# Kernel tuning notes

Hardware: AMD Instinct MI355X
Metric: run time of the kernel (lower is better)

## Reference

```python
import jax, jax.numpy as jnp
import numpy as np

EMBED = 1024
HEADS = 16
HEAD_DIM = EMBED // HEADS


def setup_inputs() -> dict:
    key = jax.random.key(0)
    ks = jax.random.split(key, 6)
    scale = 1.0 / np.sqrt(EMBED)
    x = jax.random.normal(ks[0], (2, 2048, EMBED), dtype=jnp.float32)
    # nn.Linear weights stored as [out_features, in_features]
    Wq = jax.random.normal(ks[1], (EMBED, EMBED), dtype=jnp.float32) * scale
    Wk = jax.random.normal(ks[2], (EMBED, EMBED), dtype=jnp.float32) * scale
    Wv = jax.random.normal(ks[3], (EMBED, EMBED), dtype=jnp.float32) * scale
    Wo = jax.random.normal(ks[4], (EMBED, EMBED), dtype=jnp.float32) * scale
    bo = jax.random.normal(ks[5], (EMBED,), dtype=jnp.float32) * scale
    return {"x": x, "Wq": Wq, "Wk": Wk, "Wv": Wv, "Wo": Wo, "bo": bo}


def reference(x, Wq, Wk, Wv, Wo, bo):
    N, L, E = x.shape
    # projections (torch Linear: x @ W.T)
    q = (x @ Wq.T).reshape(N, L, HEADS, HEAD_DIM).transpose(0, 2, 1, 3)  # [N,H,L,D]
    k = (x @ Wk.T).reshape(N, L, HEADS, HEAD_DIM).transpose(0, 2, 1, 3)
    v = (x @ Wv.T).reshape(N, L, HEADS, HEAD_DIM).transpose(0, 2, 1, 3)
    # scores scaled by sqrt(embed_size) (as in source, not sqrt(head_dim))
    scores = jnp.einsum("nhqd,nhkd->nhqk", q, k) / jnp.sqrt(jnp.float32(E))
    attn = jax.nn.softmax(scores, axis=-1)
    out = jnp.einsum("nhqk,nhkd->nhqd", attn, v)  # [N,H,L,D]
    out = out.transpose(0, 2, 1, 3).reshape(N, L, E)
    return out @ Wo.T + bo
```

## Files before the change

kernel.cpp:

```cpp
#include <hip/hip_runtime.h>
#include <hip/hip_bf16.h>

constexpr int NB  = 2;
constexpr int SL  = 2048;
constexpr int EMB = 1024;
constexpr int NH  = 16;
constexpr int HD  = 64;
constexpr int MT  = NB * SL;
constexpr size_t PROJ = (size_t)MT * EMB;

typedef __attribute__((ext_vector_type(8))) short bf16x8;
typedef __attribute__((ext_vector_type(4))) float f32x4;

__device__ inline short f2b(float f) {
  __hip_bfloat16 b = __float2bfloat16(f);
  short s; __builtin_memcpy(&s, &b, 2); return s;
}

#define GLDS16(g, l)                                                     \
  __builtin_amdgcn_global_load_lds(                                      \
      (const __attribute__((address_space(1))) void*)(g),                \
      (__attribute__((address_space(3))) void*)(l), 16, 0, 0)

__global__ __launch_bounds__(256) void cast_all(
    const float* __restrict__ x,  const float* __restrict__ wq,
    const float* __restrict__ wk, const float* __restrict__ wv,
    const float* __restrict__ wo, short* __restrict__ xb,
    short* __restrict__ wqkv, short* __restrict__ wob) {
  const size_t t = (size_t)blockIdx.x * 256 + threadIdx.x;
  const float* src; short* dst; size_t base;
  if (t < 1048576)      { src = x;  dst = xb;              base = 0; }
  else if (t < 1310720) { src = wq; dst = wqkv;            base = 1048576; }
  else if (t < 1572864) { src = wk; dst = wqkv + (1 << 20); base = 1310720; }
  else if (t < 1835008) { src = wv; dst = wqkv + (2 << 20); base = 1572864; }
  else                  { src = wo; dst = wob;             base = 1835008; }
  const size_t i = t - base;
  const float4 v = ((const float4*)src)[i];
  const short4 o = {f2b(v.x), f2b(v.y), f2b(v.z), f2b(v.w)};
  ((short4*)dst)[i] = o;
}

__global__ __launch_bounds__(256) void gemm_qkv(
    const short* __restrict__ A, const short* __restrict__ W,
    short* __restrict__ qb, short* __restrict__ kb, short* __restrict__ vt) {
  __shared__ short As[128 * 64];
  __shared__ short Bs[128 * 64];
  const int tid = threadIdx.x;
  const int w = tid >> 6, lane = tid & 63;
  const int la = lane >> 4, lb = lane & 15;
  const int wm = w & 1, wn = w >> 1;
  const int m0 = blockIdx.y << 7, n0 = blockIdx.x << 7;
  const int srow = lane >> 3;
  const int scol = ((lane & 7) ^ srow) << 3;
  const short* a0 = A + (size_t)(m0 + w * 32 + srow) * 1024 + scol;
  const short* b0 = W + (size_t)(n0 + w * 32 + srow) * 1024 + scol;
  short* lAw = As + (w * 32) * 64;
  short* lBw = Bs + (w * 32) * 64;

  f32x4 acc[4][4];
#pragma unroll
  for (int i = 0; i < 4; ++i)
#pragma unroll
    for (int j = 0; j < 4; ++j) acc[i][j] = (f32x4){0.f, 0.f, 0.f, 0.f};

  for (int k0 = 0; k0 < 1024; k0 += 64) {
    __syncthreads();
#pragma unroll
    for (int g = 0; g < 4; ++g) GLDS16(a0 + g * 8 * 1024 + k0, lAw + g * 8 * 64);
#pragma unroll
    for (int g = 0; g < 4; ++g) GLDS16(b0 + g * 8 * 1024 + k0, lBw + g * 8 * 64);
    __syncthreads();
#pragma unroll
    for (int ks = 0; ks < 2; ++ks) {
      bf16x8 af[4], bfr[4];
#pragma unroll
      for (int i = 0; i < 4; ++i) {
        const int row = wm * 64 + i * 16 + lb;
        af[i] = *(const bf16x8*)&As[row * 64 + (((ks << 2) + la) ^ (row & 7)) * 8];
      }
#pragma unroll
      for (int j = 0; j < 4; ++j) {
        const int row = wn * 64 + j * 16 + lb;
        bfr[j] = *(const bf16x8*)&Bs[row * 64 + (((ks << 2) + la) ^ (row & 7)) * 8];
      }
#pragma unroll
      for (int i = 0; i < 4; ++i)
#pragma unroll
        for (int j = 0; j < 4; ++j)
          acc[i][j] = __builtin_amdgcn_mfma_f32_16x16x32_bf16(af[i], bfr[j],
                                                              acc[i][j], 0, 0, 0);
    }
  }

  const int region = n0 >> 10;
  if (region == 0) {
    const float sc = 0.03125f * 1.44269504f;
#pragma unroll
    for (int j = 0; j < 4; ++j) {
      const int nj = (n0 & 1023) + wn * 64 + j * 16 + lb;
#pragma unroll
      for (int i = 0; i < 4; ++i) {
        const int mi = m0 + wm * 64 + i * 16 + la * 4;
#pragma unroll
        for (int r = 0; r < 4; ++r)
          qb[(size_t)(mi + r) * 1024 + nj] = f2b(acc[i][j][r] * sc);
      }
    }
  } else if (region == 1) {
#pragma unroll
    for (int j = 0; j < 4; ++j) {
      const int nj = (n0 & 1023) + wn * 64 + j * 16 + lb;
      const int hh = nj >> 6, d = nj & 63;
      const int ks = d >> 5, Gd = (d >> 3) & 3, jj = d & 7;
#pragma unroll
      for (int i = 0; i < 4; ++i) {
        const int mi = m0 + wm * 64 + i * 16 + la * 4;
        const int nbi = mi >> 11, seq = mi & (SL - 1);
        const size_t base = ((size_t)(nbi * NH + hh) << 17) +
                            (size_t)(seq >> 4) * 1024 + ks * 512 + Gd * 128 +
                            (seq & 15) * 8 + jj;
#pragma unroll
        for (int r = 0; r < 4; ++r) kb[base + r * 8] = f2b(acc[i][j][r]);
      }
    }
  } else {
#pragma unroll
    for (int j = 0; j < 4; ++j) {
      const int nv = (n0 - 2048) + wn * 64 + j * 16 + lb;
      const int hh = nv >> 6, d = nv & 63;
      const int mtd = d >> 4, lbv = d & 15;
#pragma unroll
      for (int i = 0; i < 4; ++i) {
        const int mi = m0 + wm * 64 + i * 16 + la * 4;
        const int nbi = mi >> 11, seq = mi & (SL - 1);
        const int kq = seq >> 5, g = (seq >> 2) & 3, hi = (seq >> 4) & 1;
        const short4 o = {f2b(acc[i][j][0]), f2b(acc[i][j][1]),
                          f2b(acc[i][j][2]), f2b(acc[i][j][3])};
        *(short4*)&vt[((size_t)(nbi * NH + hh) << 17) + (size_t)kq * 2048 +
                      mtd * 512 + g * 128 + lbv * 8 + 4 * hi] = o;
      }
    }
  }
}

__global__ __launch_bounds__(256) void gemm_out(
    const short* __restrict__ A, const short* __restrict__ W,
    const float* __restrict__ bias, float* __restrict__ out) {
  __shared__ short As[128 * 64];
  __shared__ short Bs[64 * 64];
  const int tid = threadIdx.x;
  const int w = tid >> 6, lane = tid & 63;
  const int la = lane >> 4, lb = lane & 15;
  const int wm = w & 1, wn = w >> 1;
  const int m0 = blockIdx.y << 7, n0 = blockIdx.x << 6;
  const int srow = lane >> 3;
  const int scol = ((lane & 7) ^ srow) << 3;
  const short* a0 = A + (size_t)(m0 + w * 32 + srow) * 1024 + scol;
  const short* b0 = W + (size_t)(n0 + w * 16 + srow) * 1024 + scol;
  short* lAw = As + (w * 32) * 64;
  short* lBw = Bs + (w * 16) * 64;

  f32x4 acc[4][2];
#pragma unroll
  for (int i = 0; i < 4; ++i)
#pragma unroll
    for (int j = 0; j < 2; ++j) acc[i][j] = (f32x4){0.f, 0.f, 0.f, 0.f};

  for (int k0 = 0; k0 < 1024; k0 += 64) {
    __syncthreads();
#pragma unroll
    for (int g = 0; g < 4; ++g) GLDS16(a0 + g * 8 * 1024 + k0, lAw + g * 8 * 64);
#pragma unroll
    for (int g = 0; g < 2; ++g) GLDS16(b0 + g * 8 * 1024 + k0, lBw + g * 8 * 64);
    __syncthreads();
#pragma unroll
    for (int ks = 0; ks < 2; ++ks) {
      bf16x8 af[4], bfr[2];
#pragma unroll
      for (int i = 0; i < 4; ++i) {
        const int row = wm * 64 + i * 16 + lb;
        af[i] = *(const bf16x8*)&As[row * 64 + (((ks << 2) + la) ^ (row & 7)) * 8];
      }
#pragma unroll
      for (int j = 0; j < 2; ++j) {
        const int row = wn * 32 + j * 16 + lb;
        bfr[j] = *(const bf16x8*)&Bs[row * 64 + (((ks << 2) + la) ^ (row & 7)) * 8];
      }
#pragma unroll
      for (int i = 0; i < 4; ++i)
#pragma unroll
        for (int j = 0; j < 2; ++j)
          acc[i][j] = __builtin_amdgcn_mfma_f32_16x16x32_bf16(af[i], bfr[j],
                                                              acc[i][j], 0, 0, 0);
    }
  }
#pragma unroll
  for (int j = 0; j < 2; ++j) {
    const int nj = n0 + wn * 32 + j * 16 + lb;
    const float bv = bias[nj];
#pragma unroll
    for (int i = 0; i < 4; ++i) {
      const int mi = m0 + wm * 64 + i * 16 + la * 4;
#pragma unroll
      for (int r = 0; r < 4; ++r)
        out[(size_t)(mi + r) * 1024 + nj] = acc[i][j][r] + bv;
    }
  }
}

#define LOADK(DK, KB32)                                                      \
  do {                                                                       \
    _Pragma("unroll") for (int rr_ = 0; rr_ < 2; ++rr_)                      \
        _Pragma("unroll") for (int ks_ = 0; ks_ < 2; ++ks_)                  \
            DK[rr_][ks_] = *(const bf16x8*)(Kb + (size_t)(KB32) * 2048 +     \
                                            rr_ * 1024 + ks_ * 512);         \
  } while (0)

#define LOADV(DV, KB32)                                                      \
  do {                                                                       \
    _Pragma("unroll") for (int md_ = 0; md_ < 4; ++md_)                      \
        DV[md_] = *(const bf16x8*)(Vb + (size_t)(KB32) * 2048 + md_ * 512);  \
  } while (0)

#define ATTN_STEP(AK, AV)                                                    \
  do {                                                                       \
    f32x4 S[2][4];                                                           \
    _Pragma("unroll") for (int mt = 0; mt < 2; ++mt)                         \
        _Pragma("unroll") for (int nt = 0; nt < 4; ++nt)                     \
            S[mt][nt] = (f32x4){0.f, 0.f, 0.f, 0.f};                         \
    __builtin_amdgcn_s_setprio(1);                                           \
    _Pragma("unroll") for (int ks = 0; ks < 2; ++ks)                         \
        _Pragma("unroll") for (int nt = 0; nt < 4; ++nt) {                   \
      S[0][nt] = __builtin_amdgcn_mfma_f32_16x16x32_bf16(AK[0][ks],          \
                     bQ[nt][ks], S[0][nt], 0, 0, 0);                         \
      S[1][nt] = __builtin_amdgcn_mfma_f32_16x16x32_bf16(AK[1][ks],          \
                     bQ[nt][ks], S[1][nt], 0, 0, 0);                         \
    }                                                                        \
    __builtin_amdgcn_s_setprio(0);                                           \
    _Pragma("unroll") for (int nt = 0; nt < 4; ++nt) {                       \
      _Pragma("unroll") for (int mt = 0; mt < 2; ++mt)                       \
          _Pragma("unroll") for (int r = 0; r < 4; ++r) {                    \
        const float p = __builtin_amdgcn_exp2f(S[mt][nt][r]);                \
        S[mt][nt][r] = p;                                                    \
        lacc[nt] += p;                                                       \
      }                                                                      \
      bf16x8 B2;                                                             \
      B2[0] = f2b(S[0][nt][0]); B2[1] = f2b(S[0][nt][1]);                    \
      B2[2] = f2b(S[0][nt][2]); B2[3] = f2b(S[0][nt][3]);                    \
      B2[4] = f2b(S[1][nt][0]); B2[5] = f2b(S[1][nt][1]);                    \
      B2[6] = f2b(S[1][nt][2]); B2[7] = f2b(S[1][nt][3]);                    \
      __builtin_amdgcn_s_setprio(1);                                         \
      _Pragma("unroll") for (int mtd = 0; mtd < 4; ++mtd)                    \
          O[mtd][nt] = __builtin_amdgcn_mfma_f32_16x16x32_bf16(              \
              AV[mtd], B2, O[mtd][nt], 0, 0, 0);                             \
      __builtin_amdgcn_s_setprio(0);                                         \
    }                                                                        \
  } while (0)

__global__ __launch_bounds__(256, 2) void attn_mfma(const short* __restrict__ Qg,
                                                    const short* __restrict__ Kp,
                                                    const short* __restrict__ Vp,
                                                    short* __restrict__ Ab) {
  __shared__ __align__(16) float red[2][64][68];
  __shared__ float lred[128];
  const int tid = threadIdx.x;
  const int w = tid >> 6, lane = tid & 63;
  const int G = lane >> 4, lb = lane & 15;
  const int wk = w & 1, wq = w >> 1;
  const int h = blockIdx.x, qt = blockIdx.y, n = blockIdx.z;

  const short* Qb = Qg + ((size_t)(n * SL + (qt << 7) + 64 * wq)) * EMB + h * HD;
  bf16x8 bQ[4][2];
#pragma unroll
  for (int nt = 0; nt < 4; ++nt)
#pragma unroll
    for (int ks = 0; ks < 2; ++ks)
      bQ[nt][ks] =
          *(const bf16x8*)(Qb + (size_t)(16 * nt + lb) * EMB + 32 * ks + 8 * G);

  f32x4 O[4][4];
  float lacc[4] = {0.f, 0.f, 0.f, 0.f};
#pragma unroll
  for (int i = 0; i < 4; ++i)
#pragma unroll
    for (int j = 0; j < 4; ++j) O[i][j] = (f32x4){0.f, 0.f, 0.f, 0.f};

  const short* Kb = Kp + (((size_t)(n * NH + h)) << 17) + lane * 8;
  const short* Vb = Vp + (((size_t)(n * NH + h)) << 17) + lane * 8;

  bf16x8 K0[2][2], V0[4], K1[2][2], V1[4];
  LOADK(K0, 2 * wk);
  LOADV(V0, 2 * wk);
  for (int it = 0; it < 32; it += 2) {
    const int kA = 2 * it + 2 * wk;
    LOADK(K1, kA + 1);
    LOADV(V1, kA + 1);
    ATTN_STEP(K0, V0);
    if (it + 2 < 32) {
      LOADK(K0, kA + 4);
      LOADV(V0, kA + 4);
    }
    ATTN_STEP(K1, V1);
  }

#pragma unroll
  for (int nt = 0; nt < 4; ++nt) {
    lacc[nt] += __shfl_xor(lacc[nt], 16);
    lacc[nt] += __shfl_xor(lacc[nt], 32);
  }

  if (wk == 1) {
#pragma unroll
    for (int nt = 0; nt < 4; ++nt) {
      const int q = 16 * nt + lb;
#pragma unroll
      for (int mtd = 0; mtd < 4; ++mtd)
        *(f32x4*)&red[wq][q][16 * mtd + 4 * G] = O[mtd][nt];
      if (G == 0) lred[wq * 64 + q] = lacc[nt];
    }
  }
  __syncthreads();
  if (wk == 0) {
    short* Ao = Ab + ((size_t)(n * SL + (qt << 7) + 64 * wq)) * EMB + h * HD;
#pragma unroll
    for (int nt = 0; nt < 4; ++nt) {
      const int q = 16 * nt + lb;
      const float inv = 1.f / (lacc[nt] + lred[wq * 64 + q]);
#pragma unroll
      for (int mtd = 0; mtd < 4; ++mtd) {
        const f32x4 t = *(const f32x4*)&red[wq][q][16 * mtd + 4 * G];
        const f32x4 s = t + O[mtd][nt];
        const short4 o = {f2b(s[0] * inv), f2b(s[1] * inv), f2b(s[2] * inv),
                          f2b(s[3] * inv)};
        *(short4*)(Ao + (size_t)q * EMB + 16 * mtd + 4 * G) = o;
      }
    }
  }
}

extern "C" void kernel_launch(void* const* d_in, const int* in_sizes, int n_in,
                              void* d_out, int out_size, void* d_ws, size_t ws_size,
                              hipStream_t stream) {
  const float* x  = (const float*)d_in[0];
  const float* Wq = (const float*)d_in[1];
  const float* Wk = (const float*)d_in[2];
  const float* Wv = (const float*)d_in[3];
  const float* Wo = (const float*)d_in[4];
  const float* bo = (const float*)d_in[5];
  float* out = (float*)d_out;

  short* xb   = (short*)d_ws;
  short* wqkv = xb + PROJ;
  short* wob  = wqkv + 3u * EMB * EMB;
  short* qb   = wob + (size_t)EMB * EMB;
  short* kb   = qb + PROJ;
  short* vt   = kb + PROJ;
  short* ab   = qb;

  cast_all<<<8192, 256, 0, stream>>>(x, Wq, Wk, Wv, Wo, xb, wqkv, wob);
  gemm_qkv<<<dim3(24, 32), 256, 0, stream>>>(xb, wqkv, qb, kb, vt);
  attn_mfma<<<dim3(NH, SL / 128, NB), 256, 0, stream>>>(qb, kb, vt, ab);
  gemm_out<<<dim3(16, 32), 256, 0, stream>>>(ab, wob, bo, out);
}
```

Before: 174.0 us.

## Rewrite QKV GEMM as 256x256 tile double-buffered pipeline with 8 waves

The QKV projection GEMM moves from 128x128 tiles with 4 waves and a single LDS buffer to 256x256 tiles with 8 waves, 128 KB of dynamic LDS double-buffering, and half-tile async global-to-LDS loads interleaved with MFMA groups under manual waitcnt and barriers. It also swizzles block order and raises wave priority around MFMA bursts. The aim is to hide load latency and improve operand reuse. The cost is a large LDS footprint and only 192 blocks, which may leave CUs underfilled, and the hand-placed waits carry a correctness risk.

```diff
diff --git a/kernel.cpp b/kernel.cpp
--- a/kernel.cpp
+++ b/kernel.cpp
@@ -40,56 +40,138 @@
   ((short4*)dst)[i] = o;
 }
 
-__global__ __launch_bounds__(256) void gemm_qkv(
+#define QBAR() asm volatile("s_barrier" ::: "memory")
+#define QVM(n) asm volatile("s_waitcnt vmcnt(" #n ")" ::: "memory")
+
+#define STAGEH(gh, lh)                                                   \
+  do {                                                                   \
+    GLDS16((gh) + go0, (lh) + w16 * 64);                                 \
+    GLDS16((gh) + go1, (lh) + w16 * 64 + 512);                           \
+  } while (0)
+
+#define LDAQ(pa, ks)                                                     \
+  _Pragma("unroll") for (int i_ = 0; i_ < 8; ++i_)                       \
+      aR[i_] = *(const bf16x8*)&(pa)[(wm128 + i_ * 16 + lb) * 64 +       \
+                                     ((((ks) << 2) + G) ^ lb7) * 8];
+
+#define LDBQ(dst, pb, j0, ks)                                            \
+  dst[0] = *(const bf16x8*)&(pb)[(wn64 + (j0) * 16 + lb) * 64 +          \
+                                 ((((ks) << 2) + G) ^ lb7) * 8];         \
+  dst[1] = *(const bf16x8*)&(pb)[(wn64 + ((j0) + 1) * 16 + lb) * 64 +    \
+                                 ((((ks) << 2) + G) ^ lb7) * 8];
+
+#define MMQ(bp, j0)                                                      \
+  __builtin_amdgcn_s_setprio(1);                                         \
+  _Pragma("unroll") for (int i_ = 0; i_ < 8; ++i_) {                     \
+    acc[i_][j0] = __builtin_amdgcn_mfma_f32_16x16x32_bf16(               \
+        aR[i_], bp[0], acc[i_][j0], 0, 0, 0);                            \
+    acc[i_][(j0) + 1] = __builtin_amdgcn_mfma_f32_16x16x32_bf16(         \
+        aR[i_], bp[1], acc[i_][(j0) + 1], 0, 0, 0);                      \
+  }                                                                      \
+  __builtin_amdgcn_s_setprio(0);
+
+__global__ __launch_bounds__(512, 2) void gemm_qkv(
     const short* __restrict__ A, const short* __restrict__ W,
     short* __restrict__ qb, short* __restrict__ kb, short* __restrict__ vt) {
-  __shared__ short As[128 * 64];
-  __shared__ short Bs[128 * 64];
+  extern __shared__ short lds[];
   const int tid = threadIdx.x;
   const int w = tid >> 6, lane = tid & 63;
-  const int la = lane >> 4, lb = lane & 15;
-  const int wm = w & 1, wn = w >> 1;
-  const int m0 = blockIdx.y << 7, n0 = blockIdx.x << 7;
-  const int srow = lane >> 3;
-  const int scol = ((lane & 7) ^ srow) << 3;
-  const short* a0 = A + (size_t)(m0 + w * 32 + srow) * 1024 + scol;
-  const short* b0 = W + (size_t)(n0 + w * 32 + srow) * 1024 + scol;
-  short* lAw = As + (w * 32) * 64;
-  short* lBw = Bs + (w * 32) * 64;
-
-  f32x4 acc[4][4];
-#pragma unroll
-  for (int i = 0; i < 4; ++i)
+  const int G = lane >> 4, lb = lane & 15, lb7 = lb & 7;
+  const int wm = w >> 2, wn = w & 3;
+  const int wm128 = wm * 128, wn64 = wn * 64;
+  const int bid = blockIdx.x;
+  const int swz = (bid & 7) * 24 + (bid >> 3);
+  const int by = swz / 12, bx = swz % 12;
+  const int m0 = by << 8, n0 = bx << 8;
+  const int w16 = w * 16;
+  const int lr = lane >> 3;
+  const int lc = ((lane & 7) ^ lr) << 3;
+  const size_t go0 = (size_t)(w16 + lr) * 1024 + lc;
+  const size_t go1 = go0 + (size_t)8 * 1024;
+  const short* aH0 = A + (size_t)m0 * 1024;
+  const short* aH1 = A + (size_t)(m0 + 128) * 1024;
+  const short* bH0 = W + (size_t)n0 * 1024;
+  const short* bH1 = W + (size_t)(n0 + 128) * 1024;
+  short* a0s = lds;
+  short* b0s = lds + 16384;
+  short* a1s = lds + 32768;
+  short* b1s = lds + 49152;
+
+  f32x4 acc[8][4];
+#pragma unroll
+  for (int i = 0; i < 8; ++i)
 #pragma unroll
     for (int j = 0; j < 4; ++j) acc[i][j] = (f32x4){0.f, 0.f, 0.f, 0.f};
-
-  for (int k0 = 0; k0 < 1024; k0 += 64) {
-    __syncthreads();
-#pragma unroll
-    for (int g = 0; g < 4; ++g) GLDS16(a0 + g * 8 * 1024 + k0, lAw + g * 8 * 64);
-#pragma unroll
-    for (int g = 0; g < 4; ++g) GLDS16(b0 + g * 8 * 1024 + k0, lBw + g * 8 * 64);
-    __syncthreads();
-#pragma unroll
-    for (int ks = 0; ks < 2; ++ks) {
-      bf16x8 af[4], bfr[4];
-#pragma unroll
-      for (int i = 0; i < 4; ++i) {
-        const int row = wm * 64 + i * 16 + lb;
-        af[i] = *(const bf16x8*)&As[row * 64 + (((ks << 2) + la) ^ (row & 7)) * 8];
-      }
-#pragma unroll
-      for (int j = 0; j < 4; ++j) {
-        const int row = wn * 64 + j * 16 + lb;
-        bfr[j] = *(const bf16x8*)&Bs[row * 64 + (((ks << 2) + la) ^ (row & 7)) * 8];
-      }
-#pragma unroll
-      for (int i = 0; i < 4; ++i)
-#pragma unroll
-        for (int j = 0; j < 4; ++j)
-          acc[i][j] = __builtin_amdgcn_mfma_f32_16x16x32_bf16(af[i], bfr[j],
-                                                              acc[i][j], 0, 0, 0);
-    }
+  bf16x8 aR[8], b01[2], b23[2];
+
+  STAGEH(aH0, a0s);
+  STAGEH(aH1, a0s + 8192);
+  STAGEH(bH0, b0s);
+  STAGEH(bH1, b0s + 8192);
+  STAGEH(aH0 + 64, a1s);
+  STAGEH(aH1 + 64, a1s + 8192);
+  STAGEH(bH0 + 64, b1s);
+  STAGEH(bH1 + 64, b1s + 8192);
+  QVM(8);
+  QBAR();
+
+  for (int it = 0; it < 7; ++it) {
+    const size_t k1 = (size_t)(2 * it + 1) * 64;
+    const size_t k2 = (size_t)(2 * it + 2) * 64;
+    const size_t k3 = (size_t)(2 * it + 3) * 64;
+    LDAQ(a0s, 0);
+    LDBQ(b01, b0s, 0, 0);
+    if (it > 0) STAGEH(aH1 + k1, a1s + 8192);
+    QBAR(); MMQ(b01, 0); QBAR();
+    LDBQ(b23, b0s, 2, 0);
+    if (it > 0) STAGEH(bH0 + k1, b1s);
+    QBAR(); MMQ(b23, 2); QBAR();
+    LDAQ(a0s, 1);
+    LDBQ(b01, b0s, 0, 1);
+    if (it > 0) STAGEH(bH1 + k1, b1s + 8192);
+    QBAR(); MMQ(b01, 0); QBAR();
+    LDBQ(b23, b0s, 2, 1);
+    STAGEH(aH0 + k2, a0s);
+    QVM(2);
+    QBAR(); MMQ(b23, 2); QBAR();
+    LDAQ(a1s, 0);
+    LDBQ(b01, b1s, 0, 0);
+    STAGEH(aH1 + k2, a0s + 8192);
+    QBAR(); MMQ(b01, 0); QBAR();
+    LDBQ(b23, b1s, 2, 0);
+    STAGEH(bH0 + k2, b0s);
+    QBAR(); MMQ(b23, 2); QBAR();
+    LDAQ(a1s, 1);
+    LDBQ(b01, b1s, 0, 1);
+    STAGEH(bH1 + k2, b0s + 8192);
+    QBAR(); MMQ(b01, 0); QBAR();
+    LDBQ(b23, b1s, 2, 1);
+    STAGEH(aH0 + k3, a1s);
+    QVM(2);
+    QBAR(); MMQ(b23, 2); QBAR();
+  }
+  {
+    const size_t k1 = (size_t)15 * 64;
+    LDAQ(a0s, 0); LDBQ(b01, b0s, 0, 0);
+    STAGEH(aH1 + k1, a1s + 8192);
+    QBAR(); MMQ(b01, 0); QBAR();
+    LDBQ(b23, b0s, 2, 0);
+    STAGEH(bH0 + k1, b1s);
+    QBAR(); MMQ(b23, 2); QBAR();
+    LDAQ(a0s, 1); LDBQ(b01, b0s, 0, 1);
+    STAGEH(bH1 + k1, b1s + 8192);
+    QBAR(); MMQ(b01, 0); QBAR();
+    LDBQ(b23, b0s, 2, 1);
+    QVM(0);
+    QBAR(); MMQ(b23, 2); QBAR();
+    LDAQ(a1s, 0); LDBQ(b01, b1s, 0, 0);
+    QBAR(); MMQ(b01, 0); QBAR();
+    LDBQ(b23, b1s, 2, 0);
+    QBAR(); MMQ(b23, 2); QBAR();
+    LDAQ(a1s, 1); LDBQ(b01, b1s, 0, 1);
+    QBAR(); MMQ(b01, 0); QBAR();
+    LDBQ(b23, b1s, 2, 1);
+    QBAR(); MMQ(b23, 2); QBAR();
   }
 
   const int region = n0 >> 10;
@@ -97,10 +179,10 @@
     const float sc = 0.03125f * 1.44269504f;
 #pragma unroll
     for (int j = 0; j < 4; ++j) {
-      const int nj = (n0 & 1023) + wn * 64 + j * 16 + lb;
-#pragma unroll
-      for (int i = 0; i < 4; ++i) {
-        const int mi = m0 + wm * 64 + i * 16 + la * 4;
+      const int nj = (n0 & 1023) + wn64 + j * 16 + lb;
+#pragma unroll
+      for (int i = 0; i < 8; ++i) {
+        const int mi = m0 + wm128 + i * 16 + (G << 2);
 #pragma unroll
         for (int r = 0; r < 4; ++r)
           qb[(size_t)(mi + r) * 1024 + nj] = f2b(acc[i][j][r] * sc);
@@ -109,12 +191,12 @@
   } else if (region == 1) {
 #pragma unroll
     for (int j = 0; j < 4; ++j) {
-      const int nj = (n0 & 1023) + wn * 64 + j * 16 + lb;
+      const int nj = (n0 & 1023) + wn64 + j * 16 + lb;
       const int hh = nj >> 6, d = nj & 63;
       const int ks = d >> 5, Gd = (d >> 3) & 3, jj = d & 7;
 #pragma unroll
-      for (int i = 0; i < 4; ++i) {
-        const int mi = m0 + wm * 64 + i * 16 + la * 4;
+      for (int i = 0; i < 8; ++i) {
+        const int mi = m0 + wm128 + i * 16 + (G << 2);
         const int nbi = mi >> 11, seq = mi & (SL - 1);
         const size_t base = ((size_t)(nbi * NH + hh) << 17) +
                             (size_t)(seq >> 4) * 1024 + ks * 512 + Gd * 128 +
@@ -126,12 +208,12 @@
   } else {
 #pragma unroll
     for (int j = 0; j < 4; ++j) {
-      const int nv = (n0 - 2048) + wn * 64 + j * 16 + lb;
+      const int nv = (n0 - 2048) + wn64 + j * 16 + lb;
       const int hh = nv >> 6, d = nv & 63;
       const int mtd = d >> 4, lbv = d & 15;
 #pragma unroll
-      for (int i = 0; i < 4; ++i) {
-        const int mi = m0 + wm * 64 + i * 16 + la * 4;
+      for (int i = 0; i < 8; ++i) {
+        const int mi = m0 + wm128 + i * 16 + (G << 2);
         const int nbi = mi >> 11, seq = mi & (SL - 1);
         const int kq = seq >> 5, g = (seq >> 2) & 3, hi = (seq >> 4) & 1;
         const short4 o = {f2b(acc[i][j][0]), f2b(acc[i][j][1]),
@@ -358,7 +440,7 @@
   short* ab   = qb;
 
   cast_all<<<8192, 256, 0, stream>>>(x, Wq, Wk, Wv, Wo, xb, wqkv, wob);
-  gemm_qkv<<<dim3(24, 32), 256, 0, stream>>>(xb, wqkv, qb, kb, vt);
+  gemm_qkv<<<192, 512, 131072, stream>>>(xb, wqkv, qb, kb, vt);
   attn_mfma<<<dim3(NH, SL / 128, NB), 256, 0, stream>>>(qb, kb, vt, ab);
   gemm_out<<<dim3(16, 32), 256, 0, stream>>>(ab, wob, bo, out);
 }
```

New measurement: 173.3 us. About the same (-0.4%).

## Split attention key range across four waves per query tile instead of two

Applied to the files above, without the earlier changes.

Attention blocks grow from 256 to 512 threads, so each 64-query group is handled by four waves that each cover a quarter of the keys, interleaved, instead of two waves covering halves. The partial outputs and row sums are combined through shared memory in a serial three-stage reduction with extra barriers. This raises the number of waves in flight to hide load and MFMA latency. The cost is more reduction traffic and synchronisation, and a launch bound of four 512-thread blocks per unit that tightens the register budget.

```diff
diff --git a/kernel.cpp b/kernel.cpp
--- a/kernel.cpp
+++ b/kernel.cpp
@@ -257,16 +257,16 @@
     }                                                                        \
   } while (0)
 
-__global__ __launch_bounds__(256, 2) void attn_mfma(const short* __restrict__ Qg,
+__global__ __launch_bounds__(512, 4) void attn_mfma(const short* __restrict__ Qg,
                                                     const short* __restrict__ Kp,
                                                     const short* __restrict__ Vp,
                                                     short* __restrict__ Ab) {
   __shared__ __align__(16) float red[2][64][68];
-  __shared__ float lred[128];
+  __shared__ float lred[2][64];
   const int tid = threadIdx.x;
   const int w = tid >> 6, lane = tid & 63;
   const int G = lane >> 4, lb = lane & 15;
-  const int wk = w & 1, wq = w >> 1;
+  const int wk = w & 3, wq = w >> 2;
   const int h = blockIdx.x, qt = blockIdx.y, n = blockIdx.z;
 
   const short* Qb = Qg + ((size_t)(n * SL + (qt << 7) + 64 * wq)) * EMB + h * HD;
@@ -289,16 +289,16 @@
   const short* Vb = Vp + (((size_t)(n * NH + h)) << 17) + lane * 8;
 
   bf16x8 K0[2][2], V0[4], K1[2][2], V1[4];
-  LOADK(K0, 2 * wk);
-  LOADV(V0, 2 * wk);
-  for (int it = 0; it < 32; it += 2) {
-    const int kA = 2 * it + 2 * wk;
-    LOADK(K1, kA + 1);
-    LOADV(V1, kA + 1);
+  LOADK(K0, wk);
+  LOADV(V0, wk);
+  for (int j = 0; j < 16; j += 2) {
+    const int kA = 4 * j + wk;
+    LOADK(K1, kA + 4);
+    LOADV(V1, kA + 4);
     ATTN_STEP(K0, V0);
-    if (it + 2 < 32) {
-      LOADK(K0, kA + 4);
-      LOADV(V0, kA + 4);
+    if (j + 2 < 16) {
+      LOADK(K0, kA + 8);
+      LOADV(V0, kA + 8);
     }
     ATTN_STEP(K1, V1);
   }
@@ -309,14 +309,42 @@
     lacc[nt] += __shfl_xor(lacc[nt], 32);
   }
 
-  if (wk == 1) {
+  if (wk == 3) {
 #pragma unroll
     for (int nt = 0; nt < 4; ++nt) {
       const int q = 16 * nt + lb;
 #pragma unroll
       for (int mtd = 0; mtd < 4; ++mtd)
         *(f32x4*)&red[wq][q][16 * mtd + 4 * G] = O[mtd][nt];
-      if (G == 0) lred[wq * 64 + q] = lacc[nt];
+      if (G == 0) lred[wq][q] = lacc[nt];
+    }
+  }
+  __syncthreads();
+  if (wk == 2) {
+#pragma unroll
+    for (int nt = 0; nt < 4; ++nt) {
+      const int q = 16 * nt + lb;
+#pragma unroll
+      for (int mtd = 0; mtd < 4; ++mtd) {
+        f32x4 t = *(const f32x4*)&red[wq][q][16 * mtd + 4 * G];
+        t += O[mtd][nt];
+        *(f32x4*)&red[wq][q][16 * mtd + 4 * G] = t;
+      }
+      if (G == 0) lred[wq][q] += lacc[nt];
+    }
+  }
+  __syncthreads();
+  if (wk == 1) {
+#pragma unroll
+    for (int nt = 0; nt < 4; ++nt) {
+      const int q = 16 * nt + lb;
+#pragma unroll
+      for (int mtd = 0; mtd < 4; ++mtd) {
+        f32x4 t = *(const f32x4*)&red[wq][q][16 * mtd + 4 * G];
+        t += O[mtd][nt];
+        *(f32x4*)&red[wq][q][16 * mtd + 4 * G] = t;
+      }
+      if (G == 0) lred[wq][q] += lacc[nt];
     }
   }
   __syncthreads();
@@ -325,7 +353,7 @@
 #pragma unroll
     for (int nt = 0; nt < 4; ++nt) {
       const int q = 16 * nt + lb;
-      const float inv = 1.f / (lacc[nt] + lred[wq * 64 + q]);
+      const float inv = 1.f / (lacc[nt] + lred[wq][q]);
 #pragma unroll
       for (int mtd = 0; mtd < 4; ++mtd) {
         const f32x4 t = *(const f32x4*)&red[wq][q][16 * mtd + 4 * G];
@@ -359,6 +387,6 @@
 
   cast_all<<<8192, 256, 0, stream>>>(x, Wq, Wk, Wv, Wo, xb, wqkv, wob);
   gemm_qkv<<<dim3(24, 32), 256, 0, stream>>>(xb, wqkv, qb, kb, vt);
-  attn_mfma<<<dim3(NH, SL / 128, NB), 256, 0, stream>>>(qb, kb, vt, ab);
+  attn_mfma<<<dim3(NH, SL / 128, NB), 512, 0, stream>>>(qb, kb, vt, ab);
   gemm_out<<<dim3(16, 32), 256, 0, stream>>>(ab, wob, bo, out);
 }
```

After: 532.9 us. 206% more time.

## Fuse fp32-to-bf16 casts into GEMM tile loads, dropping the cast kernel

Applied to the files above, without the earlier changes.

Removes the separate cast kernel that converted x and all weights to bf16 in workspace. The QKV and output GEMMs now stream fp32 tiles into LDS and convert to bf16 when reading MFMA fragments, with the K step halved for QKV. This drops one launch and the round trip of writing and re-reading bf16 copies. In exchange, global and LDS traffic per GEMM doubles for the fp32 operands, and x and the weights are converted repeatedly across tiles.

```diff
diff --git a/kernel.cpp b/kernel.cpp
--- a/kernel.cpp
+++ b/kernel.cpp
@@ -6,8 +6,7 @@
 constexpr int EMB = 1024;
 constexpr int NH  = 16;
 constexpr int HD  = 64;
-constexpr int MT  = NB * SL;
-constexpr size_t PROJ = (size_t)MT * EMB;
+constexpr size_t PROJ = (size_t)NB * SL * EMB;
 
 typedef __attribute__((ext_vector_type(8))) short bf16x8;
 typedef __attribute__((ext_vector_type(4))) float f32x4;
@@ -15,6 +14,13 @@
 __device__ inline short f2b(float f) {
   __hip_bfloat16 b = __float2bfloat16(f);
   short s; __builtin_memcpy(&s, &b, 2); return s;
+}
+
+__device__ inline bf16x8 pack8(f32x4 u, f32x4 v) {
+  bf16x8 r;
+  r[0] = f2b(u[0]); r[1] = f2b(u[1]); r[2] = f2b(u[2]); r[3] = f2b(u[3]);
+  r[4] = f2b(v[0]); r[5] = f2b(v[1]); r[6] = f2b(v[2]); r[7] = f2b(v[3]);
+  return r;
 }
 
 #define GLDS16(g, l)                                                     \
@@ -22,40 +28,26 @@
       (const __attribute__((address_space(1))) void*)(g),                \
       (__attribute__((address_space(3))) void*)(l), 16, 0, 0)
 
-__global__ __launch_bounds__(256) void cast_all(
-    const float* __restrict__ x,  const float* __restrict__ wq,
-    const float* __restrict__ wk, const float* __restrict__ wv,
-    const float* __restrict__ wo, short* __restrict__ xb,
-    short* __restrict__ wqkv, short* __restrict__ wob) {
-  const size_t t = (size_t)blockIdx.x * 256 + threadIdx.x;
-  const float* src; short* dst; size_t base;
-  if (t < 1048576)      { src = x;  dst = xb;              base = 0; }
-  else if (t < 1310720) { src = wq; dst = wqkv;            base = 1048576; }
-  else if (t < 1572864) { src = wk; dst = wqkv + (1 << 20); base = 1310720; }
-  else if (t < 1835008) { src = wv; dst = wqkv + (2 << 20); base = 1572864; }
-  else                  { src = wo; dst = wob;             base = 1835008; }
-  const size_t i = t - base;
-  const float4 v = ((const float4*)src)[i];
-  const short4 o = {f2b(v.x), f2b(v.y), f2b(v.z), f2b(v.w)};
-  ((short4*)dst)[i] = o;
-}
-
 __global__ __launch_bounds__(256) void gemm_qkv(
-    const short* __restrict__ A, const short* __restrict__ W,
+    const float* __restrict__ x,  const float* __restrict__ Wq,
+    const float* __restrict__ Wk, const float* __restrict__ Wv,
     short* __restrict__ qb, short* __restrict__ kb, short* __restrict__ vt) {
-  __shared__ short As[128 * 64];
-  __shared__ short Bs[128 * 64];
+  __shared__ float Asf[128 * 32];
+  __shared__ float Bsf[128 * 32];
   const int tid = threadIdx.x;
   const int w = tid >> 6, lane = tid & 63;
   const int la = lane >> 4, lb = lane & 15;
   const int wm = w & 1, wn = w >> 1;
   const int m0 = blockIdx.y << 7, n0 = blockIdx.x << 7;
+  const int region = n0 >> 10;
+  const float* Wsel = (region == 0) ? Wq : (region == 1) ? Wk : Wv;
+  const int nb0 = n0 & 1023;
   const int srow = lane >> 3;
-  const int scol = ((lane & 7) ^ srow) << 3;
-  const short* a0 = A + (size_t)(m0 + w * 32 + srow) * 1024 + scol;
-  const short* b0 = W + (size_t)(n0 + w * 32 + srow) * 1024 + scol;
-  short* lAw = As + (w * 32) * 64;
-  short* lBw = Bs + (w * 32) * 64;
+  const int scol = ((lane & 7) ^ srow) << 2;
+  const float* a0 = x + (size_t)(m0 + w * 32 + srow) * 1024 + scol;
+  const float* b0 = Wsel + (size_t)(nb0 + w * 32 + srow) * 1024 + scol;
+  float* lAw = Asf + (w * 32) * 32;
+  float* lBw = Bsf + (w * 32) * 32;
 
   f32x4 acc[4][4];
 #pragma unroll
@@ -63,41 +55,43 @@
 #pragma unroll
     for (int j = 0; j < 4; ++j) acc[i][j] = (f32x4){0.f, 0.f, 0.f, 0.f};
 
-  for (int k0 = 0; k0 < 1024; k0 += 64) {
+  for (int k0 = 0; k0 < 1024; k0 += 32) {
     __syncthreads();
 #pragma unroll
-    for (int g = 0; g < 4; ++g) GLDS16(a0 + g * 8 * 1024 + k0, lAw + g * 8 * 64);
-#pragma unroll
-    for (int g = 0; g < 4; ++g) GLDS16(b0 + g * 8 * 1024 + k0, lBw + g * 8 * 64);
+    for (int g = 0; g < 4; ++g) GLDS16(a0 + g * 8 * 1024 + k0, lAw + g * 8 * 32);
+#pragma unroll
+    for (int g = 0; g < 4; ++g) GLDS16(b0 + g * 8 * 1024 + k0, lBw + g * 8 * 32);
     __syncthreads();
-#pragma unroll
-    for (int ks = 0; ks < 2; ++ks) {
-      bf16x8 af[4], bfr[4];
-#pragma unroll
-      for (int i = 0; i < 4; ++i) {
-        const int row = wm * 64 + i * 16 + lb;
-        af[i] = *(const bf16x8*)&As[row * 64 + (((ks << 2) + la) ^ (row & 7)) * 8];
-      }
-#pragma unroll
-      for (int j = 0; j < 4; ++j) {
-        const int row = wn * 64 + j * 16 + lb;
-        bfr[j] = *(const bf16x8*)&Bs[row * 64 + (((ks << 2) + la) ^ (row & 7)) * 8];
-      }
-#pragma unroll
-      for (int i = 0; i < 4; ++i)
-#pragma unroll
-        for (int j = 0; j < 4; ++j)
-          acc[i][j] = __builtin_amdgcn_mfma_f32_16x16x32_bf16(af[i], bfr[j],
-                                                              acc[i][j], 0, 0, 0);
-    }
-  }
-
-  const int region = n0 >> 10;
+    bf16x8 af[4], bfr[4];
+#pragma unroll
+    for (int i = 0; i < 4; ++i) {
+      const int row = wm * 64 + i * 16 + lb;
+      const f32x4 u = *(const f32x4*)&Asf[row * 32 + ((2 * la) ^ (row & 7)) * 4];
+      const f32x4 v =
+          *(const f32x4*)&Asf[row * 32 + ((2 * la + 1) ^ (row & 7)) * 4];
+      af[i] = pack8(u, v);
+    }
+#pragma unroll
+    for (int j = 0; j < 4; ++j) {
+      const int row = wn * 64 + j * 16 + lb;
+      const f32x4 u = *(const f32x4*)&Bsf[row * 32 + ((2 * la) ^ (row & 7)) * 4];
+      const f32x4 v =
+          *(const f32x4*)&Bsf[row * 32 + ((2 * la + 1) ^ (row & 7)) * 4];
+      bfr[j] = pack8(u, v);
+    }
+#pragma unroll
+    for (int i = 0; i < 4; ++i)
+#pragma unroll
+      for (int j = 0; j < 4; ++j)
+        acc[i][j] = __builtin_amdgcn_mfma_f32_16x16x32_bf16(af[i], bfr[j],
+                                                            acc[i][j], 0, 0, 0);
+  }
+
   if (region == 0) {
     const float sc = 0.03125f * 1.44269504f;
 #pragma unroll
     for (int j = 0; j < 4; ++j) {
-      const int nj = (n0 & 1023) + wn * 64 + j * 16 + lb;
+      const int nj = nb0 + wn * 64 + j * 16 + lb;
 #pragma unroll
       for (int i = 0; i < 4; ++i) {
         const int mi = m0 + wm * 64 + i * 16 + la * 4;
@@ -109,7 +103,7 @@
   } else if (region == 1) {
 #pragma unroll
     for (int j = 0; j < 4; ++j) {
-      const int nj = (n0 & 1023) + wn * 64 + j * 16 + lb;
+      const int nj = nb0 + wn * 64 + j * 16 + lb;
       const int hh = nj >> 6, d = nj & 63;
       const int ks = d >> 5, Gd = (d >> 3) & 3, jj = d & 7;
 #pragma unroll
@@ -126,7 +120,7 @@
   } else {
 #pragma unroll
     for (int j = 0; j < 4; ++j) {
-      const int nv = (n0 - 2048) + wn * 64 + j * 16 + lb;
+      const int nv = nb0 + wn * 64 + j * 16 + lb;
       const int hh = nv >> 6, d = nv & 63;
       const int mtd = d >> 4, lbv = d & 15;
 #pragma unroll
@@ -144,10 +138,10 @@
 }
 
 __global__ __launch_bounds__(256) void gemm_out(
-    const short* __restrict__ A, const short* __restrict__ W,
+    const short* __restrict__ A, const float* __restrict__ Wo,
     const float* __restrict__ bias, float* __restrict__ out) {
   __shared__ short As[128 * 64];
-  __shared__ short Bs[64 * 64];
+  __shared__ float Bsf[64 * 64];
   const int tid = threadIdx.x;
   const int w = tid >> 6, lane = tid & 63;
   const int la = lane >> 4, lb = lane & 15;
@@ -156,9 +150,9 @@
   const int srow = lane >> 3;
   const int scol = ((lane & 7) ^ srow) << 3;
   const short* a0 = A + (size_t)(m0 + w * 32 + srow) * 1024 + scol;
-  const short* b0 = W + (size_t)(n0 + w * 16 + srow) * 1024 + scol;
   short* lAw = As + (w * 32) * 64;
-  short* lBw = Bs + (w * 16) * 64;
+  const int brow = lane >> 4;
+  float* lBw = Bsf + (w * 16) * 64;
 
   f32x4 acc[4][2];
 #pragma unroll
@@ -171,7 +165,13 @@
 #pragma unroll
     for (int g = 0; g < 4; ++g) GLDS16(a0 + g * 8 * 1024 + k0, lAw + g * 8 * 64);
 #pragma unroll
-    for (int g = 0; g < 2; ++g) GLDS16(b0 + g * 8 * 1024 + k0, lBw + g * 8 * 64);
+    for (int g = 0; g < 4; ++g) {
+      const int rsw = 4 * (g & 1) + brow;
+      const int bchunk = (lane & 15) ^ rsw;
+      const float* bsrc = Wo +
+          (size_t)(n0 + w * 16 + g * 4 + brow) * 1024 + k0 + bchunk * 4;
+      GLDS16(bsrc, lBw + g * 4 * 64);
+    }
     __syncthreads();
 #pragma unroll
     for (int ks = 0; ks < 2; ++ks) {
@@ -184,7 +184,11 @@
 #pragma unroll
       for (int j = 0; j < 2; ++j) {
         const int row = wn * 32 + j * 16 + lb;
-        bfr[j] = *(const bf16x8*)&Bs[row * 64 + (((ks << 2) + la) ^ (row & 7)) * 8];
+        const f32x4 u = *(const f32x4*)&Bsf[row * 64 +
+                                            ((8 * ks + 2 * la) ^ (row & 7)) * 4];
+        const f32x4 v = *(const f32x4*)&Bsf[row * 64 +
+                                            ((8 * ks + 2 * la + 1) ^ (row & 7)) * 4];
+        bfr[j] = pack8(u, v);
       }
 #pragma unroll
       for (int i = 0; i < 4; ++i)
@@ -349,16 +353,12 @@
   const float* bo = (const float*)d_in[5];
   float* out = (float*)d_out;
 
-  short* xb   = (short*)d_ws;
-  short* wqkv = xb + PROJ;
-  short* wob  = wqkv + 3u * EMB * EMB;
-  short* qb   = wob + (size_t)EMB * EMB;
-  short* kb   = qb + PROJ;
-  short* vt   = kb + PROJ;
-  short* ab   = qb;
-
-  cast_all<<<8192, 256, 0, stream>>>(x, Wq, Wk, Wv, Wo, xb, wqkv, wob);
-  gemm_qkv<<<dim3(24, 32), 256, 0, stream>>>(xb, wqkv, qb, kb, vt);
+  short* qb = (short*)d_ws;
+  short* kb = qb + PROJ;
+  short* vt = kb + PROJ;
+  short* ab = qb;
+
+  gemm_qkv<<<dim3(24, 32), 256, 0, stream>>>(x, Wq, Wk, Wv, qb, kb, vt);
   attn_mfma<<<dim3(NH, SL / 128, NB), 256, 0, stream>>>(qb, kb, vt, ab);
-  gemm_out<<<dim3(16, 32), 256, 0, stream>>>(ab, wob, bo, out);
-}
+  gemm_out<<<dim3(16, 32), 256, 0, stream>>>(ab, Wo, bo, out);
+}
```

Measured after the change: 182.5 us. 4.9% more time.
